# Kernel tuning notes

Hardware: AMD Instinct MI355X
Metric: run time of the kernel (lower is better)

The kernel has to match this reference:

```python
import jax, jax.numpy as jnp
import numpy as np

B, N, D, H = 2, 2048, 1024, 16

def setup_inputs() -> dict:
    key = jax.random.key(0)
    ks = jax.random.split(key, 5)
    X = jax.random.normal(ks[0], (B, N, D), jnp.float32)
    t_idx = jnp.sort(jax.random.randint(ks[1], (B, N), 0, 8192), axis=-1)
    attn_bool_mask = jnp.zeros((B, N, N), jnp.bool_)  # True = disallow
    Wqkv = jax.random.normal(ks[2], (3 * D, D), jnp.float32) * 0.02  # in_proj_weight
    bqkv = jnp.zeros((3 * D,), jnp.float32)
    Wo = jax.random.normal(ks[3], (D, D), jnp.float32) * 0.02  # out_proj.weight
    bo = jnp.zeros((D,), jnp.float32)
    alpha = jnp.full((H,), 0.01, jnp.float32)  # per-head recency slope
    return {"X": X, "t_idx": t_idx, "attn_bool_mask": attn_bool_mask,
            "Wqkv": Wqkv, "bqkv": bqkv, "Wo": Wo, "bo": bo, "alpha": alpha}

def reference(X, t_idx, attn_bool_mask, Wqkv, bqkv, Wo, bo, alpha):
    b, n, d = X.shape
    h = alpha.shape[0]
    hd = d // h
    # fused QKV projection (torch: X @ in_proj_weight.T + in_proj_bias)
    qkv = jnp.einsum('bnd,ed->bne', X, Wqkv) + bqkv
    q, k, v = jnp.split(qkv, 3, axis=-1)
    def to_heads(t):
        return t.reshape(b, n, h, hd).transpose(0, 2, 1, 3)  # [B,H,N,hd]
    q, k, v = to_heads(q), to_heads(k), to_heads(v)
    scores = jnp.einsum('bhqd,bhkd->bhqk', q, k) / jnp.sqrt(jnp.float32(hd))
    # recency bias: -alpha_h * max(t_q - t_k, 0), <= 0
    dqk = jnp.clip(t_idx[:, :, None] - t_idx[:, None, :], 0, None).astype(jnp.float32)
    bias = -alpha[None, :, None, None] * dqk[:, None, :, :]  # [B,H,N,N]
    bias = jnp.where(attn_bool_mask[:, None, :, :], -jnp.inf, bias)
    attn = jax.nn.softmax(scores + bias, axis=-1)
    ctx = jnp.einsum('bhqk,bhkd->bhqd', attn, v)
    ctx = ctx.transpose(0, 2, 1, 3).reshape(b, n, d)
    return jnp.einsum('bnd,ed->bne', ctx, Wo) + bo
```

## Files before the change

### kernel.cpp

```cpp
#include <hip/hip_runtime.h>
#include <hip/hip_bf16.h>


typedef __bf16 bf16;
typedef __bf16 bf16x8 __attribute__((ext_vector_type(8)));
typedef float f32x4 __attribute__((ext_vector_type(4)));

#define B_ 2
#define N_ 2048
#define D_ 1024
#define H_ 16
#define HD_ 64

#define GLL16(gp, lp)                                                      \
  __builtin_amdgcn_global_load_lds(                                        \
      (const __attribute__((address_space(1))) void*)(const void*)(gp),    \
      (__attribute__((address_space(3))) void*)(void*)(lp), 16, 0, 0)

__global__ __launch_bounds__(256) void cvt_kernel(const float* __restrict__ src,
                                                  bf16* __restrict__ dst, int n8) {
  int i = blockIdx.x * 256 + threadIdx.x;
  if (i < n8) {
    float4 a = ((const float4*)src)[2 * i];
    float4 b = ((const float4*)src)[2 * i + 1];
    bf16x8 v;
    v[0] = (bf16)a.x; v[1] = (bf16)a.y; v[2] = (bf16)a.z; v[3] = (bf16)a.w;
    v[4] = (bf16)b.x; v[5] = (bf16)b.y; v[6] = (bf16)b.z; v[7] = (bf16)b.w;
    ((bf16x8*)dst)[i] = v;
  }
}

template <int NT>
__device__ __forceinline__ void gemm_gll_core(const bf16* __restrict__ Ag,
                                              const bf16* __restrict__ Bg,
                                              f32x4 acc[4][NT]) {
  __shared__ __align__(16) bf16 lA[128 * 32];
  __shared__ __align__(16) bf16 lB[32 * NT * 32];
  const int tid = threadIdx.x;
  const int w = tid >> 6, L = tid & 63;
  const int wm = (w >> 1) * 64, wn = (w & 1) * 16 * NT;
  const int lr = L & 15, lq = L >> 4;
#pragma unroll
  for (int mt = 0; mt < 4; ++mt)
#pragma unroll
    for (int nt = 0; nt < NT; ++nt) acc[mt][nt] = (f32x4){0.f, 0.f, 0.f, 0.f};

  for (int k0 = 0; k0 < 1024; k0 += 32) {
    __syncthreads();
#pragma unroll
    for (int i = 0; i < 2; ++i) {
      int c = i * 256 + tid;
      GLL16(Ag + (c >> 2) * 1024 + k0 + (c & 3) * 8, lA + c * 8);
    }
#pragma unroll
    for (int i = 0; i < NT / 2; ++i) {
      int c = i * 256 + tid;
      GLL16(Bg + (c >> 2) * 1024 + k0 + (c & 3) * 8, lB + c * 8);
    }
    __syncthreads();
    bf16x8 af[4], bfr[NT];
#pragma unroll
    for (int mt = 0; mt < 4; ++mt)
      af[mt] = *(const bf16x8*)(lA + (wm + mt * 16 + lr) * 32 + lq * 8);
#pragma unroll
    for (int nt = 0; nt < NT; ++nt)
      bfr[nt] = *(const bf16x8*)(lB + (wn + nt * 16 + lr) * 32 + lq * 8);
#pragma unroll
    for (int mt = 0; mt < 4; ++mt)
#pragma unroll
      for (int nt = 0; nt < NT; ++nt)
        acc[mt][nt] = __builtin_amdgcn_mfma_f32_16x16x32_bf16(af[mt], bfr[nt], acc[mt][nt], 0, 0, 0);
  }
}

__global__ __launch_bounds__(256) void qkv_proj_gll(
    const bf16* __restrict__ Xb, const bf16* __restrict__ Wq, const float* __restrict__ bqkv,
    bf16* __restrict__ Qb, bf16* __restrict__ Kb, bf16* __restrict__ Vt) {
  const int bm = blockIdx.x, bn = blockIdx.y;
  f32x4 acc[4][4];
  gemm_gll_core<4>(Xb + (size_t)bm * 128 * 1024, Wq + (size_t)bn * 128 * 1024, acc);
  const int tid = threadIdx.x, w = tid >> 6, L = tid & 63;
  const int wm = (w >> 1) * 64, wn = (w & 1) * 64, lr = L & 15, lq = L >> 4;
#pragma unroll
  for (int mt = 0; mt < 4; ++mt)
#pragma unroll
    for (int nt = 0; nt < 4; ++nt)
#pragma unroll
      for (int r = 0; r < 4; ++r) {
        int m = bm * 128 + wm + mt * 16 + lq * 4 + r;
        int n = bn * 128 + wn + nt * 16 + lr;
        float v = acc[mt][nt][r] + bqkv[n];
        int sec = n >> 10, d1 = n & 1023;
        int hh = d1 >> 6, dd = d1 & 63;
        int b = m >> 11, tok = m & 2047, bh = b * H_ + hh;
        if (sec == 0)       Qb[(size_t)(bh * N_ + tok) * HD_ + dd] = (bf16)(v * 0.125f);
        else if (sec == 1)  Kb[(size_t)(bh * N_ + tok) * HD_ + dd] = (bf16)v;
        else                Vt[(size_t)(bh * HD_ + dd) * N_ + tok] = (bf16)v;
      }
}

__global__ __launch_bounds__(256) void out_proj_gll(
    const bf16* __restrict__ Ctx, const bf16* __restrict__ Wob, const float* __restrict__ bo,
    float* __restrict__ Out) {
  const int bm = blockIdx.x, bn = blockIdx.y;
  f32x4 acc[4][2];
  gemm_gll_core<2>(Ctx + (size_t)bm * 128 * 1024, Wob + (size_t)bn * 64 * 1024, acc);
  const int tid = threadIdx.x, w = tid >> 6, L = tid & 63;
  const int wm = (w >> 1) * 64, wn = (w & 1) * 32, lr = L & 15, lq = L >> 4;
#pragma unroll
  for (int mt = 0; mt < 4; ++mt)
#pragma unroll
    for (int nt = 0; nt < 2; ++nt)
#pragma unroll
      for (int r = 0; r < 4; ++r) {
        int m = bm * 128 + wm + mt * 16 + lq * 4 + r;
        int n = bn * 64 + wn + nt * 16 + lr;
        Out[(size_t)m * 1024 + n] = acc[mt][nt][r] + bo[n];
      }
}

template <bool AF32, bool BF32>
__device__ __forceinline__ void gemm128_core(const void* __restrict__ Ag_,
                                             const void* __restrict__ Bg_,
                                             f32x4 acc[4][4]) {
  __shared__ __align__(16) bf16 lA[128 * 48];
  __shared__ __align__(16) bf16 lB[128 * 48];
  const int tid = threadIdx.x;
  const int w = tid >> 6, L = tid & 63;
  const int wm = (w >> 1) * 64, wn = (w & 1) * 64;
  const int lr = L & 15, lq = L >> 4;
#pragma unroll
  for (int mt = 0; mt < 4; ++mt)
#pragma unroll
    for (int nt = 0; nt < 4; ++nt) acc[mt][nt] = (f32x4){0.f, 0.f, 0.f, 0.f};

  for (int k0 = 0; k0 < 1024; k0 += 32) {
    __syncthreads();
#pragma unroll
    for (int i = 0; i < 2; ++i) {
      int ch = i * 256 + tid;
      int row = ch >> 2, c8 = ch & 3;
      int off = row * 1024 + k0 + c8 * 8;
      if constexpr (AF32) {
        const float* A = (const float*)Ag_ + off;
        float4 a0 = *(const float4*)A;
        float4 a1 = *(const float4*)(A + 4);
        bf16x8 v;
        v[0] = (bf16)a0.x; v[1] = (bf16)a0.y; v[2] = (bf16)a0.z; v[3] = (bf16)a0.w;
        v[4] = (bf16)a1.x; v[5] = (bf16)a1.y; v[6] = (bf16)a1.z; v[7] = (bf16)a1.w;
        *(bf16x8*)(lA + row * 48 + c8 * 8) = v;
      } else {
        *(uint4*)(lA + row * 48 + c8 * 8) = *(const uint4*)((const bf16*)Ag_ + off);
      }
      if constexpr (BF32) {
        const float* Bp = (const float*)Bg_ + off;
        float4 b0 = *(const float4*)Bp;
        float4 b1 = *(const float4*)(Bp + 4);
        bf16x8 v;
        v[0] = (bf16)b0.x; v[1] = (bf16)b0.y; v[2] = (bf16)b0.z; v[3] = (bf16)b0.w;
        v[4] = (bf16)b1.x; v[5] = (bf16)b1.y; v[6] = (bf16)b1.z; v[7] = (bf16)b1.w;
        *(bf16x8*)(lB + row * 48 + c8 * 8) = v;
      } else {
        *(uint4*)(lB + row * 48 + c8 * 8) = *(const uint4*)((const bf16*)Bg_ + off);
      }
    }
    __syncthreads();
    bf16x8 af[4], bfr[4];
#pragma unroll
    for (int mt = 0; mt < 4; ++mt)
      af[mt] = *(const bf16x8*)(lA + (wm + mt * 16 + lr) * 48 + lq * 8);
#pragma unroll
    for (int nt = 0; nt < 4; ++nt)
      bfr[nt] = *(const bf16x8*)(lB + (wn + nt * 16 + lr) * 48 + lq * 8);
#pragma unroll
    for (int mt = 0; mt < 4; ++mt)
#pragma unroll
      for (int nt = 0; nt < 4; ++nt)
        acc[mt][nt] = __builtin_amdgcn_mfma_f32_16x16x32_bf16(af[mt], bfr[nt], acc[mt][nt], 0, 0, 0);
  }
}

__global__ __launch_bounds__(256) void qkv_proj_f32(
    const float* __restrict__ X, const float* __restrict__ Wqkv, const float* __restrict__ bqkv,
    bf16* __restrict__ Qb, bf16* __restrict__ Kb, bf16* __restrict__ Vt) {
  const int bm = blockIdx.x, bn = blockIdx.y;
  f32x4 acc[4][4];
  gemm128_core<true, true>(X + (size_t)bm * 128 * 1024, Wqkv + (size_t)bn * 128 * 1024, acc);
  const int tid = threadIdx.x, w = tid >> 6, L = tid & 63;
  const int wm = (w >> 1) * 64, wn = (w & 1) * 64, lr = L & 15, lq = L >> 4;
#pragma unroll
  for (int mt = 0; mt < 4; ++mt)
#pragma unroll
    for (int nt = 0; nt < 4; ++nt)
#pragma unroll
      for (int r = 0; r < 4; ++r) {
        int m = bm * 128 + wm + mt * 16 + lq * 4 + r;
        int n = bn * 128 + wn + nt * 16 + lr;
        float v = acc[mt][nt][r] + bqkv[n];
        int sec = n >> 10, d1 = n & 1023;
        int hh = d1 >> 6, dd = d1 & 63;
        int b = m >> 11, tok = m & 2047, bh = b * H_ + hh;
        if (sec == 0)       Qb[(size_t)(bh * N_ + tok) * HD_ + dd] = (bf16)(v * 0.125f);
        else if (sec == 1)  Kb[(size_t)(bh * N_ + tok) * HD_ + dd] = (bf16)v;
        else                Vt[(size_t)(bh * HD_ + dd) * N_ + tok] = (bf16)v;
      }
}

__global__ __launch_bounds__(256) void out_proj_f32(
    const bf16* __restrict__ Ctx, const float* __restrict__ Wo, const float* __restrict__ bo,
    float* __restrict__ Out) {
  const int bm = blockIdx.x, bn = blockIdx.y;
  f32x4 acc[4][4];
  gemm128_core<false, true>(Ctx + (size_t)bm * 128 * 1024, Wo + (size_t)bn * 128 * 1024, acc);
  const int tid = threadIdx.x, w = tid >> 6, L = tid & 63;
  const int wm = (w >> 1) * 64, wn = (w & 1) * 64, lr = L & 15, lq = L >> 4;
#pragma unroll
  for (int mt = 0; mt < 4; ++mt)
#pragma unroll
    for (int nt = 0; nt < 4; ++nt)
#pragma unroll
      for (int r = 0; r < 4; ++r) {
        int m = bm * 128 + wm + mt * 16 + lq * 4 + r;
        int n = bn * 128 + wn + nt * 16 + lr;
        Out[(size_t)m * 1024 + n] = acc[mt][nt][r] + bo[n];
      }
}

__global__ __launch_bounds__(256) void attn_kernel(
    const bf16* __restrict__ Qb, const bf16* __restrict__ Kb, const bf16* __restrict__ Vt,
    const int* __restrict__ t_idx, const float* __restrict__ alpha, bf16* __restrict__ Ctx) {
  __shared__ __align__(16) bf16 lK[2][64 * 64];
  __shared__ __align__(16) bf16 lV[2][64 * 64];
  __shared__ __align__(16) bf16 lP[4][16 * 64];
  __shared__ int lt[N_];
  const int tid = threadIdx.x, w = tid >> 6, L = tid & 63;
  const int lr = L & 15, lq = L >> 4;
  const int qb = blockIdx.x & 31, bh = blockIdx.x >> 5;
  const int b = bh >> 4, h = bh & 15;
  const bf16* Qp = Qb + (size_t)bh * N_ * HD_;
  const bf16* Kp = Kb + (size_t)bh * N_ * HD_;
  const bf16* Vp = Vt + (size_t)bh * HD_ * N_;
  const float alpha_h = alpha[h];
  const int q0 = qb * 64 + w * 16;

  {
    const int4* src = (const int4*)(t_idx + b * N_);
#pragma unroll
    for (int i = 0; i < 2; ++i) ((int4*)lt)[i * 256 + tid] = src[i * 256 + tid];
  }

  {
#pragma unroll
    for (int i = 0; i < 2; ++i) {
      int c = i * 256 + tid, row = c >> 3, cg = (c & 7) ^ (row & 7);
      GLL16(Kp + row * HD_ + cg * 8, lK[0] + c * 8);
      GLL16(Vp + row * N_ + cg * 8, lV[0] + c * 8);
    }
  }

  bf16x8 qf0 = *(const bf16x8*)(Qp + (q0 + lr) * HD_ + lq * 8);
  bf16x8 qf1 = *(const bf16x8*)(Qp + (q0 + lr) * HD_ + 32 + lq * 8);

  float l_i[4] = {0.f, 0.f, 0.f, 0.f};
  f32x4 accd[4];
#pragma unroll
  for (int dt = 0; dt < 4; ++dt) accd[dt] = (f32x4){0.f, 0.f, 0.f, 0.f};

  bf16* lPw = lP[w];
  float tq[4];

  for (int ic = 0; ic < N_ / 64; ++ic) {
    const int kc = ic * 64;
    const int cur = ic & 1;
    __syncthreads();
    if (ic == 0) {
      int4 tq4 = *(const int4*)(lt + q0 + lq * 4);
      tq[0] = (float)tq4.x; tq[1] = (float)tq4.y; tq[2] = (float)tq4.z; tq[3] = (float)tq4.w;
    }
    if (ic + 1 < N_ / 64) {
      const int nkc = kc + 64, nb = cur ^ 1;
#pragma unroll
      for (int i = 0; i < 2; ++i) {
        int c = i * 256 + tid, row = c >> 3, cg = (c & 7) ^ (row & 7);
        GLL16(Kp + (nkc + row) * HD_ + cg * 8, lK[nb] + c * 8);
        GLL16(Vp + row * N_ + nkc + cg * 8, lV[nb] + c * 8);
      }
    }
    f32x4 s[4];
#pragma unroll
    for (int T = 0; T < 4; ++T) {
      const bf16* kr = lK[cur] + (T * 16 + lr) * 64;
      bf16x8 kf0 = *(const bf16x8*)(kr + ((lq ^ (lr & 7)) * 8));
      bf16x8 kf1 = *(const bf16x8*)(kr + (((4 + lq) ^ (lr & 7)) * 8));
      f32x4 z = {0.f, 0.f, 0.f, 0.f};
      s[T] = __builtin_amdgcn_mfma_f32_16x16x32_bf16(qf0, kf0, z, 0, 0, 0);
      s[T] = __builtin_amdgcn_mfma_f32_16x16x32_bf16(qf1, kf1, s[T], 0, 0, 0);
    }
    float tk[4];
#pragma unroll
    for (int T = 0; T < 4; ++T) tk[T] = (float)lt[kc + T * 16 + lr];
#pragma unroll
    for (int r = 0; r < 4; ++r) {
      int q = lq * 4 + r, q7 = q & 7;
      bf16* prow = lPw + q * 64 + (lr & 7);
      float ls = 0.f;
#pragma unroll
      for (int T = 0; T < 4; ++T) {
        float sv = s[T][r] - alpha_h * fmaxf(tq[r] - tk[T], 0.f);
        float p = __expf(sv);
        ls += p;
        prow[(((T * 2) + (lr >> 3)) ^ q7) * 8] = (bf16)p;
      }
      l_i[r] += ls;
    }
    bf16x8 pf0 = *(const bf16x8*)(lPw + lr * 64 + ((lq ^ (lr & 7)) * 8));
    bf16x8 pf1 = *(const bf16x8*)(lPw + lr * 64 + (((4 + lq) ^ (lr & 7)) * 8));
#pragma unroll
    for (int dt = 0; dt < 4; ++dt) {
      const bf16* vr = lV[cur] + (dt * 16 + lr) * 64;
      bf16x8 vf0 = *(const bf16x8*)(vr + ((lq ^ (lr & 7)) * 8));
      bf16x8 vf1 = *(const bf16x8*)(vr + (((4 + lq) ^ (lr & 7)) * 8));
      accd[dt] = __builtin_amdgcn_mfma_f32_16x16x32_bf16(pf0, vf0, accd[dt], 0, 0, 0);
      accd[dt] = __builtin_amdgcn_mfma_f32_16x16x32_bf16(pf1, vf1, accd[dt], 0, 0, 0);
    }
  }

#pragma unroll
  for (int r = 0; r < 4; ++r) {
    float ls = l_i[r];
    ls += __shfl_xor(ls, 1);
    ls += __shfl_xor(ls, 2);
    ls += __shfl_xor(ls, 4);
    ls += __shfl_xor(ls, 8);
    l_i[r] = 1.f / ls;
  }
#pragma unroll
  for (int r = 0; r < 4; ++r) {
    int tok = q0 + lq * 4 + r;
#pragma unroll
    for (int dt = 0; dt < 4; ++dt)
      Ctx[(size_t)(b * N_ + tok) * D_ + h * HD_ + dt * 16 + lr] = (bf16)(accd[dt][r] * l_i[r]);
  }
}

extern "C" void kernel_launch(void* const* d_in, const int* in_sizes, int n_in,
                              void* d_out, int out_size, void* d_ws, size_t ws_size,
                              hipStream_t stream) {
  const float* X     = (const float*)d_in[0];
  const int*   t_idx = (const int*)d_in[1];
  const float* Wqkv  = (const float*)d_in[3];
  const float* bqkv  = (const float*)d_in[4];
  const float* Wo    = (const float*)d_in[5];
  const float* bo    = (const float*)d_in[6];
  const float* alpha = (const float*)d_in[7];
  float* Out = (float*)d_out;

  const size_t per = (size_t)B_ * H_ * N_ * HD_;
  const size_t nX = (size_t)B_ * N_ * D_;
  const size_t nWq = (size_t)3 * D_ * D_;
  const size_t nWo = (size_t)D_ * D_;
  const size_t needA = (nX + nWq + nWo + 4 * per) * sizeof(bf16);

  if (ws_size >= needA) {
    bf16* Xb  = (bf16*)d_ws;
    bf16* Wqb = Xb + nX;
    bf16* Wob = Wqb + nWq;
    bf16* Qb  = Wob + nWo;
    bf16* Kb  = Qb + per;
    bf16* Vt  = Kb + per;
    bf16* Ctx = Vt + per;
    cvt_kernel<<<dim3((int)(nX / 8 / 256)), 256, 0, stream>>>(X, Xb, (int)(nX / 8));
    cvt_kernel<<<dim3((int)(nWq / 8 / 256)), 256, 0, stream>>>(Wqkv, Wqb, (int)(nWq / 8));
    cvt_kernel<<<dim3((int)(nWo / 8 / 256)), 256, 0, stream>>>(Wo, Wob, (int)(nWo / 8));
    qkv_proj_gll<<<dim3(32, 24), 256, 0, stream>>>(Xb, Wqb, bqkv, Qb, Kb, Vt);
    attn_kernel<<<dim3(1024), 256, 0, stream>>>(Qb, Kb, Vt, t_idx, alpha, Ctx);
    out_proj_gll<<<dim3(32, 16), 256, 0, stream>>>(Ctx, Wob, bo, Out);
  } else {
    bf16* Qb  = (bf16*)d_ws;
    bf16* Kb  = Qb + per;
    bf16* Vt  = Kb + per;
    bf16* Ctx = Vt + per;
    qkv_proj_f32<<<dim3(32, 24), 256, 0, stream>>>(X, Wqkv, bqkv, Qb, Kb, Vt);
    attn_kernel<<<dim3(1024), 256, 0, stream>>>(Qb, Kb, Vt, t_idx, alpha, Ctx);
    out_proj_f32<<<dim3(32, 8), 256, 0, stream>>>(Ctx, Wo, bo, Out);
  }
}
```

Measured before the change: 248.9 us.

## Fuse conversions, transpose V separately, use exp2 and per-lane key permutation in attention

Merges the three fp32-to-bf16 conversion launches into one kernel. The QKV projection now writes V in row-major layout, and a new transpose kernel builds Vt with coalesced stores, replacing the scattered transposed stores in the GEMM epilogue. The attention kernel folds log2(e) into the Q scale and alpha so it can use exp2, and drops the shared t_idx staging in favour of direct vector loads. It also permutes which key rows each lane handles so P is written to LDS as bf16x4 vectors instead of scalar stores. The cost is one extra kernel launch and an extra pass over V through memory.

```diff
diff --git a/kernel.cpp b/kernel.cpp
--- a/kernel.cpp
+++ b/kernel.cpp
@@ -3,6 +3,7 @@
 
 
 typedef __bf16 bf16;
+typedef __bf16 bf16x4 __attribute__((ext_vector_type(4)));
 typedef __bf16 bf16x8 __attribute__((ext_vector_type(8)));
 typedef float f32x4 __attribute__((ext_vector_type(4)));
 
@@ -11,22 +12,52 @@
 #define D_ 1024
 #define H_ 16
 #define HD_ 64
+#define LOG2E 1.4426950408889634f
 
 #define GLL16(gp, lp)                                                      \
   __builtin_amdgcn_global_load_lds(                                        \
       (const __attribute__((address_space(1))) void*)(const void*)(gp),    \
       (__attribute__((address_space(3))) void*)(void*)(lp), 16, 0, 0)
 
-__global__ __launch_bounds__(256) void cvt_kernel(const float* __restrict__ src,
-                                                  bf16* __restrict__ dst, int n8) {
-  int i = blockIdx.x * 256 + threadIdx.x;
-  if (i < n8) {
-    float4 a = ((const float4*)src)[2 * i];
-    float4 b = ((const float4*)src)[2 * i + 1];
+__global__ __launch_bounds__(256) void cvt3_kernel(
+    const float* __restrict__ X, const float* __restrict__ Wq, const float* __restrict__ Wo,
+    bf16* __restrict__ Xb, bf16* __restrict__ Wqb, bf16* __restrict__ Wob) {
+  int blk = blockIdx.x;
+  const float* s;
+  bf16* d;
+  int base;
+  if (blk < 2048)      { s = X;  d = Xb;  base = blk; }
+  else if (blk < 3584) { s = Wq; d = Wqb; base = blk - 2048; }
+  else                 { s = Wo; d = Wob; base = blk - 3584; }
+  int i = base * 256 + threadIdx.x;
+  float4 a = ((const float4*)s)[2 * i];
+  float4 b = ((const float4*)s)[2 * i + 1];
+  bf16x8 v;
+  v[0] = (bf16)a.x; v[1] = (bf16)a.y; v[2] = (bf16)a.z; v[3] = (bf16)a.w;
+  v[4] = (bf16)b.x; v[5] = (bf16)b.y; v[6] = (bf16)b.z; v[7] = (bf16)b.w;
+  ((bf16x8*)d)[i] = v;
+}
+
+__global__ __launch_bounds__(256) void vtrans_kernel(const bf16* __restrict__ Vn,
+                                                     bf16* __restrict__ Vt) {
+  __shared__ __align__(16) bf16 lT[64 * 68];
+  const int tid = threadIdx.x;
+  const int bh = blockIdx.x >> 5, nc = (blockIdx.x & 31) * 64;
+  const bf16* src = Vn + ((size_t)bh * N_ + nc) * HD_;
+#pragma unroll
+  for (int i = 0; i < 2; ++i) {
+    int c = i * 256 + tid, row = c >> 3, c8 = c & 7;
+    *(bf16x8*)(lT + row * 68 + c8 * 8) = *(const bf16x8*)(src + row * 64 + c8 * 8);
+  }
+  __syncthreads();
+  bf16* dst = Vt + (size_t)bh * HD_ * N_ + nc;
+#pragma unroll
+  for (int i = 0; i < 2; ++i) {
+    int c = i * 256 + tid, hd = c >> 3, t8 = c & 7;
     bf16x8 v;
-    v[0] = (bf16)a.x; v[1] = (bf16)a.y; v[2] = (bf16)a.z; v[3] = (bf16)a.w;
-    v[4] = (bf16)b.x; v[5] = (bf16)b.y; v[6] = (bf16)b.z; v[7] = (bf16)b.w;
-    ((bf16x8*)dst)[i] = v;
+#pragma unroll
+    for (int j = 0; j < 8; ++j) v[j] = lT[(t8 * 8 + j) * 68 + hd];
+    *(bf16x8*)(dst + (size_t)hd * N_ + t8 * 8) = v;
   }
 }
 
@@ -75,7 +106,7 @@
 
 __global__ __launch_bounds__(256) void qkv_proj_gll(
     const bf16* __restrict__ Xb, const bf16* __restrict__ Wq, const float* __restrict__ bqkv,
-    bf16* __restrict__ Qb, bf16* __restrict__ Kb, bf16* __restrict__ Vt) {
+    bf16* __restrict__ Qb, bf16* __restrict__ Kb, bf16* __restrict__ Vn) {
   const int bm = blockIdx.x, bn = blockIdx.y;
   f32x4 acc[4][4];
   gemm_gll_core<4>(Xb + (size_t)bm * 128 * 1024, Wq + (size_t)bn * 128 * 1024, acc);
@@ -93,9 +124,10 @@
         int sec = n >> 10, d1 = n & 1023;
         int hh = d1 >> 6, dd = d1 & 63;
         int b = m >> 11, tok = m & 2047, bh = b * H_ + hh;
-        if (sec == 0)       Qb[(size_t)(bh * N_ + tok) * HD_ + dd] = (bf16)(v * 0.125f);
-        else if (sec == 1)  Kb[(size_t)(bh * N_ + tok) * HD_ + dd] = (bf16)v;
-        else                Vt[(size_t)(bh * HD_ + dd) * N_ + tok] = (bf16)v;
+        size_t idx = (size_t)(bh * N_ + tok) * HD_ + dd;
+        if (sec == 0)       Qb[idx] = (bf16)(v * (0.125f * LOG2E));
+        else if (sec == 1)  Kb[idx] = (bf16)v;
+        else                Vn[idx] = (bf16)v;
       }
 }
 
@@ -200,7 +232,7 @@
         int sec = n >> 10, d1 = n & 1023;
         int hh = d1 >> 6, dd = d1 & 63;
         int b = m >> 11, tok = m & 2047, bh = b * H_ + hh;
-        if (sec == 0)       Qb[(size_t)(bh * N_ + tok) * HD_ + dd] = (bf16)(v * 0.125f);
+        if (sec == 0)       Qb[(size_t)(bh * N_ + tok) * HD_ + dd] = (bf16)(v * (0.125f * LOG2E));
         else if (sec == 1)  Kb[(size_t)(bh * N_ + tok) * HD_ + dd] = (bf16)v;
         else                Vt[(size_t)(bh * HD_ + dd) * N_ + tok] = (bf16)v;
       }
@@ -232,7 +264,6 @@
   __shared__ __align__(16) bf16 lK[2][64 * 64];
   __shared__ __align__(16) bf16 lV[2][64 * 64];
   __shared__ __align__(16) bf16 lP[4][16 * 64];
-  __shared__ int lt[N_];
   const int tid = threadIdx.x, w = tid >> 6, L = tid & 63;
   const int lr = L & 15, lq = L >> 4;
   const int qb = blockIdx.x & 31, bh = blockIdx.x >> 5;
@@ -240,43 +271,35 @@
   const bf16* Qp = Qb + (size_t)bh * N_ * HD_;
   const bf16* Kp = Kb + (size_t)bh * N_ * HD_;
   const bf16* Vp = Vt + (size_t)bh * HD_ * N_;
-  const float alpha_h = alpha[h];
+  const int* tb = t_idx + b * N_;
+  const float a2 = alpha[h] * LOG2E;
   const int q0 = qb * 64 + w * 16;
 
-  {
-    const int4* src = (const int4*)(t_idx + b * N_);
-#pragma unroll
-    for (int i = 0; i < 2; ++i) ((int4*)lt)[i * 256 + tid] = src[i * 256 + tid];
-  }
-
-  {
-#pragma unroll
-    for (int i = 0; i < 2; ++i) {
-      int c = i * 256 + tid, row = c >> 3, cg = (c & 7) ^ (row & 7);
-      GLL16(Kp + row * HD_ + cg * 8, lK[0] + c * 8);
-      GLL16(Vp + row * N_ + cg * 8, lV[0] + c * 8);
-    }
+#pragma unroll
+  for (int i = 0; i < 2; ++i) {
+    int c = i * 256 + tid, row = c >> 3, cg = (c & 7) ^ (row & 7);
+    GLL16(Kp + row * HD_ + cg * 8, lK[0] + c * 8);
+    GLL16(Vp + row * N_ + cg * 8, lV[0] + c * 8);
   }
 
   bf16x8 qf0 = *(const bf16x8*)(Qp + (q0 + lr) * HD_ + lq * 8);
   bf16x8 qf1 = *(const bf16x8*)(Qp + (q0 + lr) * HD_ + 32 + lq * 8);
 
+  int4 tq4 = *(const int4*)(tb + q0 + lq * 4);
+  float tq[4] = {(float)tq4.x, (float)tq4.y, (float)tq4.z, (float)tq4.w};
+
   float l_i[4] = {0.f, 0.f, 0.f, 0.f};
   f32x4 accd[4];
 #pragma unroll
   for (int dt = 0; dt < 4; ++dt) accd[dt] = (f32x4){0.f, 0.f, 0.f, 0.f};
 
   bf16* lPw = lP[w];
-  float tq[4];
 
   for (int ic = 0; ic < N_ / 64; ++ic) {
     const int kc = ic * 64;
     const int cur = ic & 1;
+    int4 tk4 = *(const int4*)(tb + kc + lr * 4);
     __syncthreads();
-    if (ic == 0) {
-      int4 tq4 = *(const int4*)(lt + q0 + lq * 4);
-      tq[0] = (float)tq4.x; tq[1] = (float)tq4.y; tq[2] = (float)tq4.z; tq[3] = (float)tq4.w;
-    }
     if (ic + 1 < N_ / 64) {
       const int nkc = kc + 64, nb = cur ^ 1;
 #pragma unroll
@@ -289,37 +312,38 @@
     f32x4 s[4];
 #pragma unroll
     for (int T = 0; T < 4; ++T) {
-      const bf16* kr = lK[cur] + (T * 16 + lr) * 64;
-      bf16x8 kf0 = *(const bf16x8*)(kr + ((lq ^ (lr & 7)) * 8));
-      bf16x8 kf1 = *(const bf16x8*)(kr + (((4 + lq) ^ (lr & 7)) * 8));
+      int rk = 4 * lr + T, r7 = rk & 7;
+      const bf16* kr = lK[cur] + rk * 64;
+      bf16x8 kf0 = *(const bf16x8*)(kr + ((lq ^ r7) * 8));
+      bf16x8 kf1 = *(const bf16x8*)(kr + (((lq ^ 4) ^ r7) * 8));
       f32x4 z = {0.f, 0.f, 0.f, 0.f};
       s[T] = __builtin_amdgcn_mfma_f32_16x16x32_bf16(qf0, kf0, z, 0, 0, 0);
       s[T] = __builtin_amdgcn_mfma_f32_16x16x32_bf16(qf1, kf1, s[T], 0, 0, 0);
     }
-    float tk[4];
-#pragma unroll
-    for (int T = 0; T < 4; ++T) tk[T] = (float)lt[kc + T * 16 + lr];
+    float tk[4] = {(float)tk4.x, (float)tk4.y, (float)tk4.z, (float)tk4.w};
 #pragma unroll
     for (int r = 0; r < 4; ++r) {
-      int q = lq * 4 + r, q7 = q & 7;
-      bf16* prow = lPw + q * 64 + (lr & 7);
+      bf16x4 pb;
       float ls = 0.f;
 #pragma unroll
       for (int T = 0; T < 4; ++T) {
-        float sv = s[T][r] - alpha_h * fmaxf(tq[r] - tk[T], 0.f);
-        float p = __expf(sv);
+        float sv = s[T][r] - a2 * fmaxf(tq[r] - tk[T], 0.f);
+        float p = __builtin_amdgcn_exp2f(sv);
         ls += p;
-        prow[(((T * 2) + (lr >> 3)) ^ q7) * 8] = (bf16)p;
+        pb[T] = (bf16)p;
       }
       l_i[r] += ls;
+      int bS = (lr >> 1) ^ r ^ ((lq & 1) << 2);
+      *(bf16x4*)(lPw + (lq * 4 + r) * 64 + bS * 8 + (lr & 1) * 4) = pb;
     }
     bf16x8 pf0 = *(const bf16x8*)(lPw + lr * 64 + ((lq ^ (lr & 7)) * 8));
-    bf16x8 pf1 = *(const bf16x8*)(lPw + lr * 64 + (((4 + lq) ^ (lr & 7)) * 8));
+    bf16x8 pf1 = *(const bf16x8*)(lPw + lr * 64 + (((lq ^ 4) ^ (lr & 7)) * 8));
 #pragma unroll
     for (int dt = 0; dt < 4; ++dt) {
-      const bf16* vr = lV[cur] + (dt * 16 + lr) * 64;
-      bf16x8 vf0 = *(const bf16x8*)(vr + ((lq ^ (lr & 7)) * 8));
-      bf16x8 vf1 = *(const bf16x8*)(vr + (((4 + lq) ^ (lr & 7)) * 8));
+      int rv = dt * 16 + lr, r7 = rv & 7;
+      const bf16* vr = lV[cur] + rv * 64;
+      bf16x8 vf0 = *(const bf16x8*)(vr + ((lq ^ r7) * 8));
+      bf16x8 vf1 = *(const bf16x8*)(vr + (((lq ^ 4) ^ r7) * 8));
       accd[dt] = __builtin_amdgcn_mfma_f32_16x16x32_bf16(pf0, vf0, accd[dt], 0, 0, 0);
       accd[dt] = __builtin_amdgcn_mfma_f32_16x16x32_bf16(pf1, vf1, accd[dt], 0, 0, 0);
     }
@@ -369,10 +393,10 @@
     bf16* Kb  = Qb + per;
     bf16* Vt  = Kb + per;
     bf16* Ctx = Vt + per;
-    cvt_kernel<<<dim3((int)(nX / 8 / 256)), 256, 0, stream>>>(X, Xb, (int)(nX / 8));
-    cvt_kernel<<<dim3((int)(nWq / 8 / 256)), 256, 0, stream>>>(Wqkv, Wqb, (int)(nWq / 8));
-    cvt_kernel<<<dim3((int)(nWo / 8 / 256)), 256, 0, stream>>>(Wo, Wob, (int)(nWo / 8));
-    qkv_proj_gll<<<dim3(32, 24), 256, 0, stream>>>(Xb, Wqb, bqkv, Qb, Kb, Vt);
+    bf16* Vn  = Ctx;
+    cvt3_kernel<<<dim3(4096), 256, 0, stream>>>(X, Wqkv, Wo, Xb, Wqb, Wob);
+    qkv_proj_gll<<<dim3(32, 24), 256, 0, stream>>>(Xb, Wqb, bqkv, Qb, Kb, Vn);
+    vtrans_kernel<<<dim3(1024), 256, 0, stream>>>(Vn, Vt);
     attn_kernel<<<dim3(1024), 256, 0, stream>>>(Qb, Kb, Vt, t_idx, alpha, Ctx);
     out_proj_gll<<<dim3(32, 16), 256, 0, stream>>>(Ctx, Wob, bo, Out);
   } else {
```

Result: faster. 227.1 us (-8.8%).
